# Optimization experiments

Hardware: AMD Instinct MI355X
Metric: run time of the kernel (lower is better)

The kernel has to match this reference:

```python
import jax, jax.numpy as jnp
import numpy as np

B, L, EMB, H, NL, E, MAXA, PAD = 64, 512, 400, 256, 3, 512, 32, 0


def setup_inputs() -> dict:
    key = jax.random.key(0)
    ks = jax.random.split(key, 12)
    s = lambda k, shape: jax.random.normal(k, shape, jnp.float32) * 0.02
    Semb = jax.random.normal(ks[0], (B, EMB, L), jnp.float32)
    word_ids = jax.random.randint(ks[1], (B, L), 0, 30000)
    y1 = jax.random.randint(ks[2], (B,), 0, L - MAXA)
    span = jax.random.randint(ks[3], (B,), 0, MAXA)
    y2 = y1 + span
    edges = jax.random.randint(ks[4], (B, E, 2), 0, L)
    return dict(
        Semb=Semb,
        ans_sent_word_ids=word_ids,
        y1_in_sent=y1,
        y2_in_sent=y2,
        edges=edges,
        W1=s(ks[5], (H, EMB)),                 # Initialized_Conv1d (k=1, no bias)
        hw_lin_W=s(ks[6], (2, H, H)), hw_lin_b=jnp.zeros((2, H), jnp.float32),
        hw_gate_W=s(ks[7], (2, H, H)), hw_gate_b=jnp.zeros((2, H), jnp.float32),
        gcn_W=s(ks[8], (NL, H, H)), gcn_b=jnp.zeros((NL, H), jnp.float32),
        conv_W=s(ks[9], (1, NL * H)), conv_b=jnp.zeros((1,), jnp.float32),
        lin_W=s(ks[10], (L, L)), lin_b=jnp.zeros((L,), jnp.float32),
    )


def reference(Semb, ans_sent_word_ids, y1_in_sent, y2_in_sent, edges,
              W1, hw_lin_W, hw_lin_b, hw_gate_W, hw_gate_b,
              gcn_W, gcn_b, conv_W, conv_b, lin_W, lin_b):
    # 1x1 conv: [B, EMB, L] -> [B, H, L]
    x = jnp.einsum('oi,bit->bot', W1, Semb)
    # 2-layer Highway (dropout is identity in eval)
    for i in range(2):
        gate = jax.nn.sigmoid(jnp.einsum('oi,bit->bot', hw_gate_W[i], x) + hw_gate_b[i][None, :, None])
        nonlin = jnp.einsum('oi,bit->bot', hw_lin_W[i], x) + hw_lin_b[i][None, :, None]
        x = gate * nonlin + (1.0 - gate) * x
    maskS = (ans_sent_word_ids != PAD).astype(x.dtype)            # [B, L]
    # answer-span mask (Aemb itself is dead code in the original forward's output)
    pos = y1_in_sent[:, None] + jnp.arange(MAXA)                   # [B, MAXA]
    maskA = (pos <= y2_in_sent[:, None]).astype(x.dtype)
    # dense adjacency from edge list (undirected since gcn_directed=False)
    bidx = jnp.broadcast_to(jnp.arange(B)[:, None], (B, E))
    adj = jnp.zeros((B, L, L), x.dtype)
    adj = adj.at[bidx, edges[..., 0], edges[..., 1]].set(1.0)
    adj = adj.at[bidx, edges[..., 1], edges[..., 0]].set(1.0)
    # GCN (C-GCN style: W(Ax) + W(x), note bias counted twice, /(deg+1), relu)
    h = x.transpose(0, 2, 1)                                       # [B, L, H]
    denom = jnp.sum(adj, axis=2, keepdims=True) + 1.0              # [B, L, 1]
    outs = []
    for l in range(NL):
        Ax = jnp.einsum('bls,bsh->blh', adj, h)
        AxW = jnp.einsum('blh,oh->blo', Ax + h, gcn_W[l]) + 2.0 * gcn_b[l]
        h = jax.nn.relu(AxW / denom)
        outs.append(h)
    cat = jnp.concatenate(outs, axis=2)                            # [B, L, NL*H]
    y = jax.nn.relu(jnp.einsum('blc,oc->bol', cat, conv_W) + conv_b[None, :, None])  # [B,1,L]
    logits = (jnp.einsum('bol,ml->bom', y, lin_W) + lin_b).squeeze(1)                # [B,L]
    logits = logits * maskS + (1.0 - maskS) * (-1e30)
    return (logits, maskA)
```

## Files before the change

### kernel.cpp

```cpp
#include <hip/hip_runtime.h>
#include <cstdint>

#define B 64
#define L 512
#define EMB 400
#define KPAD 416
#define H 256
#define NL 3
#define NE 512
#define MAXA 32
#define M_TOT (B * L)

typedef unsigned short u16;
typedef float f32x4 __attribute__((ext_vector_type(4)));
typedef short short8 __attribute__((ext_vector_type(8)));
typedef u16 u16x8 __attribute__((ext_vector_type(8)));

__device__ __forceinline__ float b2f(u16 u) {
  unsigned v = ((unsigned)u) << 16;
  return __builtin_bit_cast(float, v);
}
__device__ __forceinline__ u16 f2b(float f) {
  unsigned u = __builtin_bit_cast(unsigned, f);
  unsigned r = (u + 0x7fffu + ((u >> 16) & 1u)) >> 16;
  return (u16)r;
}

#define GL16(g, l)                                                              \
  __builtin_amdgcn_global_load_lds((const __attribute__((address_space(1))) void*)(g), \
                                   (__attribute__((address_space(3))) void*)(l), 16, 0, 0)

template <int EPI>
__global__ __launch_bounds__(256, 2) void gemm64(
    const u16* __restrict__ A, const u16* __restrict__ Bw, const u16* __restrict__ B2w,
    const int K,
    const float* __restrict__ bias1, const float* __restrict__ bias2,
    const float* __restrict__ rden, const float* __restrict__ cw,
    float* __restrict__ yv, u16* __restrict__ Out) {
  constexpr bool HW = (EPI == 1);
  __shared__ u16 Bl0[256 * 32];
  __shared__ u16 Bl1[256 * 32];
  __shared__ u16 Al0[64 * 32];
  __shared__ u16 Al1[64 * 32];
  __shared__ u16 Cl0[HW ? 256 * 32 : 8];
  __shared__ u16 Cl1[HW ? 256 * 32 : 8];

  const int t = threadIdx.x;
  const int wid = t >> 6, lane = t & 63;
  const int m0 = blockIdx.x * 64;
  const int fr = lane & 15, kg = lane >> 4;
  const int r4 = t >> 2, ksg = t & 3;

  f32x4 acc[4][4] = {};
  f32x4 acc2[4][4] = {};

  auto stage = [&](u16* Ab, u16* Bb, u16* Cb, int kk) {
    const int kc = kk * 32 + ksg * 8;
#pragma unroll
    for (int c = 0; c < 4; ++c)
      GL16(Bw + (size_t)(c * 64 + r4) * K + kc, Bb + (size_t)(c * 256 + wid * 64) * 8);
    if constexpr (HW) {
#pragma unroll
      for (int c = 0; c < 4; ++c)
        GL16(B2w + (size_t)(c * 64 + r4) * K + kc, Cb + (size_t)(c * 256 + wid * 64) * 8);
    }
    GL16(A + (size_t)(m0 + r4) * K + kc, Ab + (size_t)(wid * 64) * 8);
  };
  auto compute = [&](const u16* Ab, const u16* Bb, const u16* Cb) {
    short8 af[4], bf[4], cf[4];
#pragma unroll
    for (int i = 0; i < 4; ++i) {
      af[i] = *(const short8*)(Ab + ((size_t)(i * 16 + fr) * 4 + kg) * 8);
      bf[i] = *(const short8*)(Bb + ((size_t)(wid * 64 + i * 16 + fr) * 4 + kg) * 8);
      if constexpr (HW)
        cf[i] = *(const short8*)(Cb + ((size_t)(wid * 64 + i * 16 + fr) * 4 + kg) * 8);
    }
#pragma unroll
    for (int mi = 0; mi < 4; ++mi)
#pragma unroll
      for (int ni = 0; ni < 4; ++ni) {
        acc[mi][ni] = __builtin_amdgcn_mfma_f32_16x16x32_bf16(af[mi], bf[ni], acc[mi][ni], 0, 0, 0);
        if constexpr (HW)
          acc2[mi][ni] =
              __builtin_amdgcn_mfma_f32_16x16x32_bf16(af[mi], cf[ni], acc2[mi][ni], 0, 0, 0);
      }
  };

  const int nk = K >> 5;
  stage(Al0, Bl0, Cl0, 0);
  for (int kk = 0; kk < nk; ++kk) {
    u16* Ac = (kk & 1) ? Al1 : Al0;
    u16* Bc = (kk & 1) ? Bl1 : Bl0;
    u16* Cc = (kk & 1) ? Cl1 : Cl0;
    u16* An = (kk & 1) ? Al0 : Al1;
    u16* Bn = (kk & 1) ? Bl0 : Bl1;
    u16* Cn = (kk & 1) ? Cl0 : Cl1;
    if (kk + 1 < nk) {
      stage(An, Bn, Cn, kk + 1);
      if constexpr (HW)
        asm volatile("s_waitcnt vmcnt(9)" ::: "memory");
      else
        asm volatile("s_waitcnt vmcnt(5)" ::: "memory");
    } else {
      asm volatile("s_waitcnt vmcnt(0)" ::: "memory");
    }
    __builtin_amdgcn_s_barrier();
    asm volatile("" ::: "memory");
    compute(Ac, Bc, Cc);
    __builtin_amdgcn_s_barrier();
    asm volatile("" ::: "memory");
  }

  const int r0 = kg * 4;
  const int c0 = wid * 64 + fr;
  if constexpr (EPI == 0) {
#pragma unroll
    for (int ni = 0; ni < 4; ++ni) {
      const int col = c0 + ni * 16;
#pragma unroll
      for (int mi = 0; mi < 4; ++mi)
#pragma unroll
        for (int rr = 0; rr < 4; ++rr)
          Out[(size_t)(m0 + mi * 16 + r0 + rr) * H + col] = f2b(acc[mi][ni][rr]);
    }
  } else if constexpr (EPI == 1) {
#pragma unroll
    for (int ni = 0; ni < 4; ++ni) {
      const int col = c0 + ni * 16;
      const float b1 = bias1[col], b2 = bias2[col];
#pragma unroll
      for (int mi = 0; mi < 4; ++mi)
#pragma unroll
        for (int rr = 0; rr < 4; ++rr) {
          const int row = m0 + mi * 16 + r0 + rr;
          const float g = 1.f / (1.f + __expf(-(acc[mi][ni][rr] + b1)));
          const float nn = acc2[mi][ni][rr] + b2;
          const float x = b2f(A[(size_t)row * K + col]);
          Out[(size_t)row * H + col] = f2b(g * nn + (1.f - g) * x);
        }
    }
  } else {
    float ypart[16];
#pragma unroll
    for (int q = 0; q < 16; ++q) ypart[q] = 0.f;
#pragma unroll
    for (int ni = 0; ni < 4; ++ni) {
      const int col = c0 + ni * 16;
      const float b1 = 2.f * bias1[col];
      const float cwv = cw[col];
#pragma unroll
      for (int mi = 0; mi < 4; ++mi)
#pragma unroll
        for (int rr = 0; rr < 4; ++rr) {
          const int row = m0 + mi * 16 + r0 + rr;
          const float s = (acc[mi][ni][rr] + b1) * rden[row];
          const float rl = s > 0.f ? s : 0.f;
          ypart[mi * 4 + rr] += rl * cwv;
          if constexpr (EPI == 2) Out[(size_t)row * H + col] = f2b(rl);
        }
    }
#pragma unroll
    for (int q = 0; q < 16; ++q) {
      float p = ypart[q];
      p += __shfl_xor(p, 1);
      p += __shfl_xor(p, 2);
      p += __shfl_xor(p, 4);
      p += __shfl_xor(p, 8);
      if (fr == 0) atomicAdd(&yv[m0 + (q >> 2) * 16 + r0 + (q & 3)], p);
    }
  }
}

__global__ __launch_bounds__(256) void k_gather(const unsigned* __restrict__ bm,
                                                const u16* __restrict__ h,
                                                u16* __restrict__ T) {
  const int t = threadIdx.x;
  const int tok = blockIdx.x * 8 + (t >> 5);
  const int b = tok >> 9;
  const int c = (t & 31) * 8;
  const uint4* wp4 = (const uint4*)(bm + (size_t)tok * 16);
  const uint4 w0 = wp4[0], w1 = wp4[1], w2 = wp4[2], w3 = wp4[3];
  const unsigned wa[16] = {w0.x, w0.y, w0.z, w0.w, w1.x, w1.y, w1.z, w1.w,
                           w2.x, w2.y, w2.z, w2.w, w3.x, w3.y, w3.z, w3.w};
  float acc[8];
  {
    const u16x8 v = *(const u16x8*)(h + (size_t)tok * H + c);
#pragma unroll
    for (int i = 0; i < 8; ++i) acc[i] = b2f(v[i]);
  }
#pragma unroll
  for (int wi = 0; wi < 16; ++wi) {
    unsigned bits = wa[wi];
    while (bits) {
      const int bit = __ffs(bits) - 1;
      bits &= bits - 1;
      const int s = wi * 32 + bit;
      const u16x8 u = *(const u16x8*)(h + (size_t)(b * L + s) * H + c);
#pragma unroll
      for (int i = 0; i < 8; ++i) acc[i] += b2f(u[i]);
    }
  }
  u16x8 o;
#pragma unroll
  for (int i = 0; i < 8; ++i) o[i] = f2b(acc[i]);
  *(u16x8*)(T + (size_t)tok * H + c) = o;
}

__global__ void k_zero(uint4* __restrict__ p) {
  p[blockIdx.x * 256 + threadIdx.x] = uint4{0, 0, 0, 0};
}

__global__ void k_edges(const int* __restrict__ edges, unsigned* __restrict__ bm) {
  const int t = blockIdx.x * 256 + threadIdx.x;
  const int b = t >> 9, e = t & 511;
  const int u = edges[(size_t)(b * NE + e) * 2 + 0];
  const int v = edges[(size_t)(b * NE + e) * 2 + 1];
  atomicOr(&bm[(size_t)(b * L + u) * 16 + (v >> 5)], 1u << (v & 31));
  atomicOr(&bm[(size_t)(b * L + v) * 16 + (u >> 5)], 1u << (u & 31));
}

#define NSEMBT (B * 56)
__global__ __launch_bounds__(256) void k_prep(const float* __restrict__ Semb,
                                              const float* __restrict__ W1,
                                              const float* __restrict__ gW,
                                              const float* __restrict__ lW,
                                              const float* __restrict__ gcnW,
                                              const unsigned* __restrict__ bm,
                                              u16* __restrict__ A0,
                                              u16* __restrict__ W1b, u16* __restrict__ HWGb,
                                              u16* __restrict__ HWLb, u16* __restrict__ GCNb,
                                              float* __restrict__ rden) {
  const int t = threadIdx.x;
  if (blockIdx.x < NSEMBT) {
    const int bid = blockIdx.x;
    const int b = bid / 56, rem = bid - b * 56;
    const int e0 = (rem >> 3) * 64, l0 = (rem & 7) * 64;
    __shared__ u16 tile[64][72];
    {
      const int er = t >> 2, ls = (t & 3) * 16;
      if (e0 + er < EMB) {
        const float* src = Semb + ((size_t)b * EMB + e0 + er) * L + l0 + ls;
#pragma unroll
        for (int i = 0; i < 4; ++i) {
          const float4 v = *(const float4*)(src + i * 4);
          tile[er][ls + i * 4 + 0] = f2b(v.x);
          tile[er][ls + i * 4 + 1] = f2b(v.y);
          tile[er][ls + i * 4 + 2] = f2b(v.z);
          tile[er][ls + i * 4 + 3] = f2b(v.w);
        }
      } else {
#pragma unroll
        for (int i = 0; i < 16; ++i) tile[er][ls + i] = 0;
      }
    }
    __syncthreads();
    {
      const int lr = t >> 2, es = (t & 3) * 16;
      if (e0 + es < KPAD) {
        u16x8 v0, v1;
#pragma unroll
        for (int i = 0; i < 8; ++i) v0[i] = tile[es + i][lr];
#pragma unroll
        for (int i = 0; i < 8; ++i) v1[i] = tile[es + 8 + i][lr];
        u16* dst = A0 + (size_t)(b * L + l0 + lr) * KPAD + e0 + es;
        *(u16x8*)dst = v0;
        *(u16x8*)(dst + 8) = v1;
      }
    }
    return;
  }
  int i = (blockIdx.x - NSEMBT) * 256 + t;
  if (i < 256 * KPAD) {
    const int o = i / KPAD, k = i - o * KPAD;
    W1b[i] = (k < EMB) ? f2b(W1[o * EMB + k]) : (u16)0;
    return;
  }
  i -= 256 * KPAD;
  if (i < 2 * H * H) { HWGb[i] = f2b(gW[i]); return; }
  i -= 2 * H * H;
  if (i < 2 * H * H) { HWLb[i] = f2b(lW[i]); return; }
  i -= 2 * H * H;
  if (i < NL * H * H) { GCNb[i] = f2b(gcnW[i]); return; }
  i -= NL * H * H;
  if (i < M_TOT) {
    const uint4* p = (const uint4*)(bm + (size_t)i * 16);
    int c = 0;
#pragma unroll
    for (int w = 0; w < 4; ++w) {
      const uint4 v = p[w];
      c += __popc(v.x) + __popc(v.y) + __popc(v.z) + __popc(v.w);
    }
    rden[i] = 1.f / (1.f + (float)c);
  }
}

__global__ __launch_bounds__(256) void k_logits(const float* __restrict__ yv,
                                                const float* __restrict__ cb,
                                                const float* __restrict__ lw,
                                                const float* __restrict__ lb,
                                                const int* __restrict__ wids,
                                                const int* __restrict__ y1,
                                                const int* __restrict__ y2,
                                                float* __restrict__ out) {
  if (blockIdx.x == B * 2) {
#pragma unroll
    for (int j = 0; j < 8; ++j) {
      const int idx = j * 256 + threadIdx.x;
      const int b = idx >> 5, q = idx & 31;
      out[B * L + idx] = (y1[b] + q <= y2[b]) ? 1.0f : 0.0f;
    }
    return;
  }
  const int b = blockIdx.x >> 1;
  const int m = ((blockIdx.x & 1) << 8) + threadIdx.x;
  __shared__ float ys[512];
  const float cb0 = cb[0];
  ys[threadIdx.x] = fmaxf(yv[(size_t)b * L + threadIdx.x] + cb0, 0.f);
  ys[threadIdx.x + 256] = fmaxf(yv[(size_t)b * L + 256 + threadIdx.x] + cb0, 0.f);
  __syncthreads();
  float acc = lb[m];
  const float4* wr = (const float4*)(lw + (size_t)m * L);
#pragma unroll 4
  for (int l4 = 0; l4 < 128; ++l4) {
    const float4 w4 = wr[l4];
    acc += ys[l4 * 4] * w4.x + ys[l4 * 4 + 1] * w4.y + ys[l4 * 4 + 2] * w4.z +
           ys[l4 * 4 + 3] * w4.w;
  }
  out[(size_t)b * L + m] = (wids[(size_t)b * L + m] != 0) ? acc : -1.0e30f;
}

extern "C" void kernel_launch(void* const* d_in, const int* in_sizes, int n_in,
                              void* d_out, int out_size, void* d_ws, size_t ws_size,
                              hipStream_t stream) {
  (void)in_sizes; (void)n_in; (void)out_size; (void)ws_size;
  const float* Semb      = (const float*)d_in[0];
  const int*   wids      = (const int*)d_in[1];
  const int*   y1        = (const int*)d_in[2];
  const int*   y2        = (const int*)d_in[3];
  const int*   edges     = (const int*)d_in[4];
  const float* W1        = (const float*)d_in[5];
  const float* hw_lin_W  = (const float*)d_in[6];
  const float* hw_lin_b  = (const float*)d_in[7];
  const float* hw_gate_W = (const float*)d_in[8];
  const float* hw_gate_b = (const float*)d_in[9];
  const float* gcn_W     = (const float*)d_in[10];
  const float* gcn_b     = (const float*)d_in[11];
  const float* conv_W    = (const float*)d_in[12];
  const float* conv_b    = (const float*)d_in[13];
  const float* lin_W     = (const float*)d_in[14];
  const float* lin_b     = (const float*)d_in[15];
  float* out = (float*)d_out;

  char* ws = (char*)d_ws;
  const size_t SZA = (size_t)M_TOT * KPAD * 2;
  const size_t SZX = (size_t)M_TOT * H * 2;
  u16* A0   = (u16*)(ws);
  u16* P0b  = (u16*)(ws + SZA);
  u16* P1b  = (u16*)(ws + SZA + SZX);
  u16* O0   = (u16*)(ws + SZA + 2 * SZX);
  u16* O1   = (u16*)(ws + SZA + 3 * SZX);
  char* wp  = ws + SZA + 4 * SZX;
  u16* W1b  = (u16*)(wp);
  u16* HWGb = (u16*)(wp + 212992);
  u16* HWLb = (u16*)(wp + 212992 + 262144);
  u16* GCNb = (u16*)(wp + 212992 + 2 * 262144);
  char* sp  = wp + 212992 + 2 * 262144 + 393216;
  unsigned* bm   = (unsigned*)(sp);
  float*    yv   = (float*)(sp + 2097152);
  float*    rden = (float*)(sp + 2097152 + 131072);

  k_zero<<<dim3(544), 256, 0, stream>>>((uint4*)bm);
  k_edges<<<dim3(B * NE / 256), 256, 0, stream>>>(edges, bm);

  const int ncvt = 256 * KPAD + 4 * H * H + NL * H * H + M_TOT;
  k_prep<<<dim3(NSEMBT + (ncvt + 255) / 256), 256, 0, stream>>>(
      Semb, W1, hw_gate_W, hw_lin_W, gcn_W, bm, A0, W1b, HWGb, HWLb, GCNb, rden);

  gemm64<0><<<dim3(M_TOT / 64), 256, 0, stream>>>(A0, W1b, nullptr, KPAD, nullptr, nullptr,
                                                  nullptr, nullptr, nullptr, P0b);
  gemm64<1><<<dim3(M_TOT / 64), 256, 0, stream>>>(P0b, HWGb, HWLb, H, hw_gate_b, hw_lin_b,
                                                  nullptr, nullptr, nullptr, P1b);
  gemm64<1><<<dim3(M_TOT / 64), 256, 0, stream>>>(P1b, HWGb + H * H, HWLb + H * H, H,
                                                  hw_gate_b + H, hw_lin_b + H, nullptr, nullptr,
                                                  nullptr, P0b);
  k_gather<<<dim3(M_TOT / 8), 256, 0, stream>>>(bm, P0b, P1b);
  gemm64<2><<<dim3(M_TOT / 64), 256, 0, stream>>>(P1b, GCNb, nullptr, H, gcn_b, nullptr,
                                                  rden, conv_W, yv, O0);
  k_gather<<<dim3(M_TOT / 8), 256, 0, stream>>>(bm, O0, P0b);
  gemm64<2><<<dim3(M_TOT / 64), 256, 0, stream>>>(P0b, GCNb + H * H, nullptr, H, gcn_b + H,
                                                  nullptr, rden, conv_W + H, yv, O1);
  k_gather<<<dim3(M_TOT / 8), 256, 0, stream>>>(bm, O1, P1b);
  gemm64<3><<<dim3(M_TOT / 64), 256, 0, stream>>>(P1b, GCNb + 2 * H * H, nullptr, H,
                                                  gcn_b + 2 * H, nullptr, rden,
                                                  conv_W + 2 * H, yv, nullptr);

  k_logits<<<dim3(B * 2 + 1), 256, 0, stream>>>(yv, conv_b, lin_W, lin_b, wids, y1, y2, out);
}
```

Baseline: 180.9 us.

## Fuse Semb transpose/convert into the 1x1 conv GEMM, dropping A0 buffer

A new k_convT kernel loads each 64-token fp32 Semb tile, converts it to bf16 and transposes it into shared memory in the MFMA fragment layout, then runs the K=416 GEMM against W1 directly. This removes the separate transpose pass in k_prep and the round trip through the bf16 A0 workspace in global memory. The cost is that the new GEMM does not pipeline B loads (it waits on vmcnt(0) every k-step), and the large shared-memory footprint (about 69KB) may limit occupancy.

```diff
diff --git a/kernel.cpp b/kernel.cpp
--- a/kernel.cpp
+++ b/kernel.cpp
@@ -29,6 +29,98 @@
 #define GL16(g, l)                                                              \
   __builtin_amdgcn_global_load_lds((const __attribute__((address_space(1))) void*)(g), \
                                    (__attribute__((address_space(3))) void*)(l), 16, 0, 0)
+
+__global__ __launch_bounds__(256, 2) void k_convT(const float* __restrict__ Semb,
+                                                  const u16* __restrict__ W1b,
+                                                  u16* __restrict__ Out) {
+  __shared__ u16 smem[64 * KPAD + 256 * 32];
+  u16* At = smem;
+  u16* Bt = smem + 64 * KPAD;
+  u16 (*tmp)[72] = (u16(*)[72])Bt;
+
+  const int t = threadIdx.x;
+  const int wid = t >> 6, lane = t & 63;
+  const int m0 = blockIdx.x * 64;
+  const int b = m0 >> 9, l0 = m0 & 511;
+  const int fr = lane & 15, kg = lane >> 4;
+  const int r4 = t >> 2, ksg = t & 3;
+
+  for (int et = 0; et < 7; ++et) {
+    const int e0 = et * 64;
+    const int erows = (et < 6) ? 64 : 32;
+    {
+      const int er = t >> 2, ls = (t & 3) * 16;
+      if (er < erows) {
+        if (e0 + er < EMB) {
+          const float* src = Semb + ((size_t)b * EMB + e0 + er) * L + l0 + ls;
+#pragma unroll
+          for (int i = 0; i < 4; ++i) {
+            const float4 v = *(const float4*)(src + i * 4);
+            tmp[er][ls + i * 4 + 0] = f2b(v.x);
+            tmp[er][ls + i * 4 + 1] = f2b(v.y);
+            tmp[er][ls + i * 4 + 2] = f2b(v.z);
+            tmp[er][ls + i * 4 + 3] = f2b(v.w);
+          }
+        } else {
+#pragma unroll
+          for (int i = 0; i < 16; ++i) tmp[er][ls + i] = 0;
+        }
+      }
+    }
+    __syncthreads();
+    {
+      const int lr = t >> 2, es = (t & 3) * 16;
+      if (es < erows) {
+        u16x8 v0, v1;
+#pragma unroll
+        for (int i = 0; i < 8; ++i) v0[i] = tmp[es + i][lr];
+#pragma unroll
+        for (int i = 0; i < 8; ++i) v1[i] = tmp[es + 8 + i][lr];
+        const int k = e0 + es;
+        u16* dst = At + (((size_t)(k >> 5) * 64 + lr) * 4 + ((k & 31) >> 3)) * 8;
+        *(u16x8*)dst = v0;
+        *(u16x8*)(dst + 8) = v1;
+      }
+    }
+    __syncthreads();
+  }
+
+  f32x4 acc[4][4] = {};
+  for (int kk = 0; kk < (KPAD >> 5); ++kk) {
+    const int kc = kk * 32 + ksg * 8;
+#pragma unroll
+    for (int c = 0; c < 4; ++c)
+      GL16(W1b + (size_t)(c * 64 + r4) * KPAD + kc, Bt + (size_t)(c * 256 + wid * 64) * 8);
+    asm volatile("s_waitcnt vmcnt(0)" ::: "memory");
+    __builtin_amdgcn_s_barrier();
+    asm volatile("" ::: "memory");
+    short8 af[4], bf[4];
+#pragma unroll
+    for (int i = 0; i < 4; ++i) {
+      af[i] = *(const short8*)(At + ((size_t)(kk * 64 + i * 16 + fr) * 4 + kg) * 8);
+      bf[i] = *(const short8*)(Bt + ((size_t)(wid * 64 + i * 16 + fr) * 4 + kg) * 8);
+    }
+#pragma unroll
+    for (int mi = 0; mi < 4; ++mi)
+#pragma unroll
+      for (int ni = 0; ni < 4; ++ni)
+        acc[mi][ni] = __builtin_amdgcn_mfma_f32_16x16x32_bf16(af[mi], bf[ni], acc[mi][ni], 0, 0, 0);
+    __builtin_amdgcn_s_barrier();
+    asm volatile("" ::: "memory");
+  }
+
+  const int r0 = kg * 4;
+  const int c0 = wid * 64 + fr;
+#pragma unroll
+  for (int ni = 0; ni < 4; ++ni) {
+    const int col = c0 + ni * 16;
+#pragma unroll
+    for (int mi = 0; mi < 4; ++mi)
+#pragma unroll
+      for (int rr = 0; rr < 4; ++rr)
+        Out[(size_t)(m0 + mi * 16 + r0 + rr) * H + col] = f2b(acc[mi][ni][rr]);
+  }
+}
 
 template <int EPI>
 __global__ __launch_bounds__(256, 2) void gemm64(
@@ -113,17 +205,7 @@
 
   const int r0 = kg * 4;
   const int c0 = wid * 64 + fr;
-  if constexpr (EPI == 0) {
-#pragma unroll
-    for (int ni = 0; ni < 4; ++ni) {
-      const int col = c0 + ni * 16;
-#pragma unroll
-      for (int mi = 0; mi < 4; ++mi)
-#pragma unroll
-        for (int rr = 0; rr < 4; ++rr)
-          Out[(size_t)(m0 + mi * 16 + r0 + rr) * H + col] = f2b(acc[mi][ni][rr]);
-    }
-  } else if constexpr (EPI == 1) {
+  if constexpr (EPI == 1) {
 #pragma unroll
     for (int ni = 0; ni < 4; ++ni) {
       const int col = c0 + ni * 16;
@@ -219,57 +301,13 @@
   atomicOr(&bm[(size_t)(b * L + v) * 16 + (u >> 5)], 1u << (u & 31));
 }
 
-#define NSEMBT (B * 56)
-__global__ __launch_bounds__(256) void k_prep(const float* __restrict__ Semb,
-                                              const float* __restrict__ W1,
-                                              const float* __restrict__ gW,
-                                              const float* __restrict__ lW,
-                                              const float* __restrict__ gcnW,
-                                              const unsigned* __restrict__ bm,
-                                              u16* __restrict__ A0,
-                                              u16* __restrict__ W1b, u16* __restrict__ HWGb,
-                                              u16* __restrict__ HWLb, u16* __restrict__ GCNb,
-                                              float* __restrict__ rden) {
-  const int t = threadIdx.x;
-  if (blockIdx.x < NSEMBT) {
-    const int bid = blockIdx.x;
-    const int b = bid / 56, rem = bid - b * 56;
-    const int e0 = (rem >> 3) * 64, l0 = (rem & 7) * 64;
-    __shared__ u16 tile[64][72];
-    {
-      const int er = t >> 2, ls = (t & 3) * 16;
-      if (e0 + er < EMB) {
-        const float* src = Semb + ((size_t)b * EMB + e0 + er) * L + l0 + ls;
-#pragma unroll
-        for (int i = 0; i < 4; ++i) {
-          const float4 v = *(const float4*)(src + i * 4);
-          tile[er][ls + i * 4 + 0] = f2b(v.x);
-          tile[er][ls + i * 4 + 1] = f2b(v.y);
-          tile[er][ls + i * 4 + 2] = f2b(v.z);
-          tile[er][ls + i * 4 + 3] = f2b(v.w);
-        }
-      } else {
-#pragma unroll
-        for (int i = 0; i < 16; ++i) tile[er][ls + i] = 0;
-      }
-    }
-    __syncthreads();
-    {
-      const int lr = t >> 2, es = (t & 3) * 16;
-      if (e0 + es < KPAD) {
-        u16x8 v0, v1;
-#pragma unroll
-        for (int i = 0; i < 8; ++i) v0[i] = tile[es + i][lr];
-#pragma unroll
-        for (int i = 0; i < 8; ++i) v1[i] = tile[es + 8 + i][lr];
-        u16* dst = A0 + (size_t)(b * L + l0 + lr) * KPAD + e0 + es;
-        *(u16x8*)dst = v0;
-        *(u16x8*)(dst + 8) = v1;
-      }
-    }
-    return;
-  }
-  int i = (blockIdx.x - NSEMBT) * 256 + t;
+__global__ void k_prep(const float* __restrict__ W1, const float* __restrict__ gW,
+                       const float* __restrict__ lW, const float* __restrict__ gcnW,
+                       const unsigned* __restrict__ bm,
+                       u16* __restrict__ W1b, u16* __restrict__ HWGb,
+                       u16* __restrict__ HWLb, u16* __restrict__ GCNb,
+                       float* __restrict__ rden) {
+  int i = blockIdx.x * 256 + threadIdx.x;
   if (i < 256 * KPAD) {
     const int o = i / KPAD, k = i - o * KPAD;
     W1b[i] = (k < EMB) ? f2b(W1[o * EMB + k]) : (u16)0;
@@ -352,14 +390,12 @@
   float* out = (float*)d_out;
 
   char* ws = (char*)d_ws;
-  const size_t SZA = (size_t)M_TOT * KPAD * 2;
   const size_t SZX = (size_t)M_TOT * H * 2;
-  u16* A0   = (u16*)(ws);
-  u16* P0b  = (u16*)(ws + SZA);
-  u16* P1b  = (u16*)(ws + SZA + SZX);
-  u16* O0   = (u16*)(ws + SZA + 2 * SZX);
-  u16* O1   = (u16*)(ws + SZA + 3 * SZX);
-  char* wp  = ws + SZA + 4 * SZX;
+  u16* P0b  = (u16*)(ws);
+  u16* P1b  = (u16*)(ws + SZX);
+  u16* O0   = (u16*)(ws + 2 * SZX);
+  u16* O1   = (u16*)(ws + 3 * SZX);
+  char* wp  = ws + 4 * SZX;
   u16* W1b  = (u16*)(wp);
   u16* HWGb = (u16*)(wp + 212992);
   u16* HWLb = (u16*)(wp + 212992 + 262144);
@@ -373,11 +409,11 @@
   k_edges<<<dim3(B * NE / 256), 256, 0, stream>>>(edges, bm);
 
   const int ncvt = 256 * KPAD + 4 * H * H + NL * H * H + M_TOT;
-  k_prep<<<dim3(NSEMBT + (ncvt + 255) / 256), 256, 0, stream>>>(
-      Semb, W1, hw_gate_W, hw_lin_W, gcn_W, bm, A0, W1b, HWGb, HWLb, GCNb, rden);
-
-  gemm64<0><<<dim3(M_TOT / 64), 256, 0, stream>>>(A0, W1b, nullptr, KPAD, nullptr, nullptr,
-                                                  nullptr, nullptr, nullptr, P0b);
+  k_prep<<<dim3((ncvt + 255) / 256), 256, 0, stream>>>(W1, hw_gate_W, hw_lin_W, gcn_W, bm,
+                                                       W1b, HWGb, HWLb, GCNb, rden);
+
+  k_convT<<<dim3(M_TOT / 64), 256, 0, stream>>>(Semb, W1b, P0b);
+
   gemm64<1><<<dim3(M_TOT / 64), 256, 0, stream>>>(P0b, HWGb, HWLb, H, hw_gate_b, hw_lin_b,
                                                   nullptr, nullptr, nullptr, P1b);
   gemm64<1><<<dim3(M_TOT / 64), 256, 0, stream>>>(P1b, HWGb + H * H, HWLb + H * H, H,
```

Measured after the change: 174.3 us. -3.6%, faster.
